# Optimization experiments

Measured on AMD Instinct MI355X. Metric: run time of the kernel, lower is better.

## Reference

```python
import jax, jax.numpy as jnp
import numpy as np

N = 50000
E = 1_000_000
IN_F = 128
NRELA = 128
OUT_F = 128
ALPHA = 0.2  # LeakyReLU negative slope


def setup_inputs() -> dict:
    key = jax.random.key(0)
    k1, k2, k3, k4, k5 = jax.random.split(key, 5)
    inp = {
        "input": jax.random.normal(k1, (N, IN_F), dtype=jnp.float32),
        "edge_embed": jax.random.normal(k2, (E, NRELA), dtype=jnp.float32),
        # xavier_normal-ish scale for the attention params
        "a": jax.random.normal(k3, (OUT_F, 2 * IN_F + NRELA), dtype=jnp.float32) * 0.08,
        "a_2": jax.random.normal(k4, (1, OUT_F), dtype=jnp.float32) * 0.15,
        "edge": jax.random.randint(k5, (2, E), 0, N, dtype=jnp.int64),
    }
    return inp


def reference(input, edge_embed, a, a_2, edge):
    n = input.shape[0]
    src = edge[0]  # aggregation key (row index of sparse tensor)
    dst = edge[1]
    # edge_h: [E, 2*in + nrela]
    edge_h = jnp.concatenate([input[src], input[dst], edge_embed], axis=1)
    # edge_m: [E, out]  (original computes a @ edge_h.T -> [out, E])
    edge_m = edge_h @ a.T
    # powers: [E]
    powers = -jax.nn.leaky_relu(edge_m @ a_2[0], negative_slope=ALPHA)
    edge_e = jnp.exp(powers)  # [E]
    # rowsum over edges sharing the same source node: [N]
    e_rowsum = jax.ops.segment_sum(edge_e, src, num_segments=n)
    e_rowsum = jnp.where(e_rowsum == 0.0, 1e-12, e_rowsum)
    # weighted aggregation: [N, out]
    edge_w = edge_e[:, None] * edge_m
    h_prime = jax.ops.segment_sum(edge_w, src, num_segments=n)
    h_prime = h_prime / e_rowsum[:, None]
    return jax.nn.elu(h_prime)  # concat=True path
```

## Files before the change

### kernel.cpp

```cpp
#include <hip/hip_runtime.h>
#include <math.h>

namespace {

typedef __attribute__((ext_vector_type(8))) short short8;
typedef __attribute__((ext_vector_type(4))) float f32x4;
typedef __attribute__((ext_vector_type(2))) float f2v;

__device__ inline unsigned short f2bf(float x) {
    unsigned u = __float_as_uint(x);
    unsigned r = (u + 0x7FFF + ((u >> 16) & 1)) >> 16;
    return (unsigned short)r;
}

__device__ inline f2v nt2(const f2v* p) { return __builtin_nontemporal_load(p); }
__device__ inline long long ntll(const long long* p) { return __builtin_nontemporal_load(p); }

__device__ inline float wave_sum64(float x) {
    int t;
    t = __builtin_amdgcn_update_dpp(0, __float_as_int(x), 0x111, 0xf, 0xf, true);
    x += __int_as_float(t);
    t = __builtin_amdgcn_update_dpp(0, __float_as_int(x), 0x112, 0xf, 0xf, true);
    x += __int_as_float(t);
    t = __builtin_amdgcn_update_dpp(0, __float_as_int(x), 0x114, 0xf, 0xf, true);
    x += __int_as_float(t);
    t = __builtin_amdgcn_update_dpp(0, __float_as_int(x), 0x118, 0xf, 0xf, true);
    x += __int_as_float(t);
    t = __builtin_amdgcn_update_dpp(0, __float_as_int(x), 0x142, 0xa, 0xf, true);
    x += __int_as_float(t);
    t = __builtin_amdgcn_update_dpp(0, __float_as_int(x), 0x143, 0xc, 0xf, true);
    x += __int_as_float(t);
    return __int_as_float(__builtin_amdgcn_readlane(__float_as_int(x), 63));
}

__global__ void kprep(const int* __restrict__ edge, const float* __restrict__ a,
                      const float* __restrict__ a2, int* __restrict__ flag,
                      unsigned short* __restrict__ Bp12, unsigned short* __restrict__ Bp3,
                      float* __restrict__ w3) {
    int tid = blockIdx.x * blockDim.x + threadIdx.x;
    if (tid < 32768) {
        int j = tid & 7, l = (tid >> 3) & 63, s = (tid >> 9) & 3, f = tid >> 11;
        int col = f * 16 + (l & 15);
        int k = s * 32 + ((l >> 4) << 3) + j;
        float v = (col < 128) ? a[col * 384 + k] : a[(col - 128) * 384 + 128 + k];
        Bp12[tid] = f2bf(v);
    }
    if (tid < 16384) {
        int j = tid & 7, l = (tid >> 3) & 63, s = (tid >> 9) & 3, f = tid >> 11;
        int col = f * 16 + (l & 15);
        int k = s * 32 + ((l >> 4) << 3) + j;
        Bp3[tid] = f2bf(a[col * 384 + 256 + k]);
    }
    if (blockIdx.x == 0 && threadIdx.x < 64) {
        int hw = edge[2 * threadIdx.x + 1];
        unsigned long long b = __ballot(hw == 0);
        if (threadIdx.x == 0) *flag = (b == ~0ull) ? 1 : 0;
    }
    if (blockIdx.x == 1 && threadIdx.x < 128) {
        int k = threadIdx.x;
        float s = 0.f;
        for (int j = 0; j < 128; ++j) s += a2[j] * a[j * 384 + 256 + k];
        w3[k] = s;
    }
}

__global__ __launch_bounds__(256) void kA(const float* __restrict__ input,
                                          const unsigned short* __restrict__ Bp,
                                          const float* __restrict__ a2,
                                          float* __restrict__ U,
                                          unsigned short* __restrict__ Vb,
                                          float* __restrict__ su, float* __restrict__ sv,
                                          const int* __restrict__ edge,
                                          const int* __restrict__ flag,
                                          int* __restrict__ counts,
                                          int n, int E, int nb1) {
    __shared__ char Asb[16384];
    if (blockIdx.x >= nb1) {
        bool is64 = (*flag != 0);
        int half = E >> 1;
        int stride = 1024 * 256;
        for (int i = (blockIdx.x - nb1) * 256 + threadIdx.x; i < half; i += stride) {
            int s0, s1;
            if (is64) { int4 v = ((const int4*)edge)[i]; s0 = v.x; s1 = v.z; }
            else      { int2 v = ((const int2*)edge)[i]; s0 = v.x; s1 = v.y; }
            atomicAdd(&counts[s0], 1);
            atomicAdd(&counts[s1], 1);
        }
        if ((E & 1) && blockIdx.x == nb1 && threadIdx.x == 0) {
            int i = E - 1;
            int s = is64 ? edge[2 * (size_t)i] : edge[i];
            atomicAdd(&counts[s], 1);
        }
        return;
    }
    int tid = threadIdx.x;
    int wid = tid >> 6, lane = tid & 63;
    int rb = blockIdx.x * 64;
    const float4* inp4 = (const float4*)input;
    for (int it = tid; it < 2048; it += 256) {
        int row = it >> 5, c4 = it & 31;
        int gr = rb + row;
        float4 v = make_float4(0.f, 0.f, 0.f, 0.f);
        if (gr < n) v = inp4[(size_t)gr * 32 + c4];
        unsigned long long pk = (unsigned long long)f2bf(v.x) |
                                ((unsigned long long)f2bf(v.y) << 16) |
                                ((unsigned long long)f2bf(v.z) << 32) |
                                ((unsigned long long)f2bf(v.w) << 48);
        int byte = (row * 256 + c4 * 8) ^ ((row & 7) << 4);
        *(unsigned long long*)(Asb + byte) = pk;
    }
    __syncthreads();

    f32x4 acc[16];
    #pragma unroll
    for (int f = 0; f < 16; ++f) acc[f] = (f32x4){0.f, 0.f, 0.f, 0.f};
    const short8* Bf = (const short8*)Bp;
    int arow = (wid << 4) | (lane & 15);
    int abase = arow * 256 + ((lane >> 4) << 4);
    int xorv = (arow & 7) << 4;
    #pragma unroll
    for (int s = 0; s < 4; ++s) {
        short8 af = *(const short8*)(Asb + ((abase + s * 64) ^ xorv));
        #pragma unroll
        for (int f = 0; f < 16; ++f)
            acc[f] = __builtin_amdgcn_mfma_f32_16x16x32_bf16(af, Bf[(f * 4 + s) * 64 + lane],
                                                             acc[f], 0, 0, 0);
    }

    int rloc = (wid << 4) + ((lane >> 4) << 2);
    int cb = lane & 15;
    #pragma unroll
    for (int f = 0; f < 16; ++f) {
        int col = f * 16 + cb;
        #pragma unroll
        for (int reg = 0; reg < 4; ++reg) {
            int r = rb + rloc + reg;
            if (r < n) {
                if (col < 128) U[(size_t)r * 128 + col] = acc[f][reg];
                else           Vb[(size_t)r * 128 + (col - 128)] = f2bf(acc[f][reg]);
            }
        }
    }

    float coef[8];
    #pragma unroll
    for (int f = 0; f < 8; ++f) coef[f] = a2[f * 16 + cb];
    #pragma unroll
    for (int reg = 0; reg < 4; ++reg) {
        float pu = 0.f, pv = 0.f;
        #pragma unroll
        for (int f = 0; f < 8; ++f) {
            pu += acc[f][reg] * coef[f];
            pv += acc[f + 8][reg] * coef[f];
        }
        #pragma unroll
        for (int off = 1; off < 16; off <<= 1) {
            pu += __shfl_xor(pu, off);
            pv += __shfl_xor(pv, off);
        }
        int r = rb + rloc + reg;
        if (cb == 0 && r < n) { su[r] = pu; sv[r] = pv; }
    }
}

__global__ __launch_bounds__(1024) void k3a(int* __restrict__ counts,
                                            int* __restrict__ row_start,
                                            int* __restrict__ partials, int n) {
    __shared__ int wsum[16];
    int tid = threadIdx.x;
    int i = blockIdx.x * 1024 + tid;
    int lane = tid & 63, wv = tid >> 6;
    int v = 0;
    if (i < n) { v = counts[i]; counts[i] = 0; }
    int x = v;
    #pragma unroll
    for (int off = 1; off < 64; off <<= 1) {
        int t = __shfl_up(x, off);
        if (lane >= off) x += t;
    }
    if (lane == 63) wsum[wv] = x;
    __syncthreads();
    if (wv == 0) {
        int ws = (lane < 16) ? wsum[lane] : 0;
        #pragma unroll
        for (int off = 1; off < 16; off <<= 1) {
            int t = __shfl_up(ws, off);
            if (lane >= off) ws += t;
        }
        if (lane < 16) wsum[lane] = ws;
    }
    __syncthreads();
    int woff = (wv > 0) ? wsum[wv - 1] : 0;
    if (i < n) row_start[i] = woff + x - v;
    if (tid == 1023) partials[blockIdx.x] = wsum[15];
}

__global__ void k3b(const int* __restrict__ partials, int* __restrict__ poffs,
                    int* __restrict__ row_start, int nb, int n) {
    int lane = threadIdx.x;
    int carry = 0;
    for (int base = 0; base < nb; base += 64) {
        int v = (base + lane < nb) ? partials[base + lane] : 0;
        int x = v;
        #pragma unroll
        for (int off = 1; off < 64; off <<= 1) {
            int t = __shfl_up(x, off);
            if (lane >= off) x += t;
        }
        if (base + lane < nb) poffs[base + lane] = carry + x - v;
        carry += __shfl(x, 63);
    }
    if (lane == 0) row_start[n] = carry;
}

__global__ void k4_scatter(const int* __restrict__ edge, const int* __restrict__ flag,
                           const int* __restrict__ row_start, const int* __restrict__ poffs,
                           int* __restrict__ counts, long long* __restrict__ epack, int E) {
    bool is64 = (*flag != 0);
    int half = E >> 1;
    int stride = gridDim.x * blockDim.x;
    const int* dbase = edge + (is64 ? 2 * (size_t)E : (size_t)E);
    for (int i = blockIdx.x * blockDim.x + threadIdx.x; i < half; i += stride) {
        int s0, s1, d0, d1;
        if (is64) {
            int4 v = ((const int4*)edge)[i];  s0 = v.x; s1 = v.z;
            int4 w = ((const int4*)dbase)[i]; d0 = w.x; d1 = w.z;
        } else {
            int2 v = ((const int2*)edge)[i];  s0 = v.x; s1 = v.y;
            int2 w = ((const int2*)dbase)[i]; d0 = w.x; d1 = w.y;
        }
        int p0 = row_start[s0] + poffs[s0 >> 10] + atomicAdd(&counts[s0], 1);
        epack[p0] = (long long)(unsigned)(2 * i) | ((long long)(unsigned)d0 << 32);
        int p1 = row_start[s1] + poffs[s1 >> 10] + atomicAdd(&counts[s1], 1);
        epack[p1] = (long long)(unsigned)(2 * i + 1) | ((long long)(unsigned)d1 << 32);
    }
    if ((E & 1) && blockIdx.x == 0 && threadIdx.x == 0) {
        int i = E - 1;
        int s = is64 ? edge[2 * (size_t)i] : edge[i];
        int d = is64 ? dbase[2 * (size_t)i] : dbase[i];
        int pos = row_start[s] + poffs[s >> 10] + atomicAdd(&counts[s], 1);
        epack[pos] = (long long)(unsigned)i | ((long long)(unsigned)d << 32);
    }
}

__global__ __launch_bounds__(256, 3) void k5_agg(const float* __restrict__ edge_embed,
                                                 const unsigned short* __restrict__ Vb,
                                                 const float* __restrict__ su,
                                                 const float* __restrict__ sv,
                                                 const float* __restrict__ w3,
                                                 const int* __restrict__ row_start,
                                                 const int* __restrict__ poffs,
                                                 const long long* __restrict__ epack,
                                                 float* __restrict__ T, float* __restrict__ W,
                                                 float* __restrict__ rowsum, int n) {
    int w = (int)(((size_t)blockIdx.x * blockDim.x + threadIdx.x) >> 6);
    int lane = threadIdx.x & 63;
    if (w >= n) return;
    int start = row_start[w] + poffs[w >> 10];
    int end = (w + 1 < n) ? (row_start[w + 1] + poffs[(w + 1) >> 10]) : row_start[n];
    f2v w3v = ((const f2v*)w3)[lane];
    float su_n = su[w];
    const f2v* EE = (const f2v*)edge_embed;
    const unsigned* VV = (const unsigned*)Vb;
    f2v Tacc = 0.f, Wacc = 0.f;
    float rs = 0.f;
    long long eds[8];
    #pragma unroll
    for (int i = 0; i < 8; ++i)
        eds[i] = (start + i < end) ? ntll(&epack[start + i]) : 0;
    for (int e0 = start; e0 < end; e0 += 8) {
        int nb = end - e0;
        if (nb > 8) nb = 8;
        long long edsn[8];
        #pragma unroll
        for (int i = 0; i < 8; ++i) {
            int idx = e0 + 8 + i;
            edsn[i] = (idx < end) ? ntll(&epack[idx]) : 0;
        }
        f2v emb[8], vv[8];
        float svv[8], part[8];
        #pragma unroll
        for (int i = 0; i < 8; ++i) {
            if (i < nb) {
                int eid = (int)eds[i];
                int dst = (int)(eds[i] >> 32);
                emb[i] = nt2(EE + (size_t)eid * 64 + lane);
                unsigned pv = VV[(size_t)dst * 64 + lane];
                vv[i].x = __uint_as_float(pv << 16);
                vv[i].y = __uint_as_float(pv & 0xffff0000u);
                svv[i] = sv[dst];
            } else {
                emb[i] = 0.f; vv[i] = 0.f; svv[i] = 0.f;
            }
        }
        #pragma unroll
        for (int i = 0; i < 8; ++i)
            part[i] = wave_sum64(emb[i].x * w3v.x + emb[i].y * w3v.y);
        #pragma unroll
        for (int i = 0; i < 8; ++i) {
            if (i < nb) {
                float s = su_n + svv[i] + part[i];
                float lr = (s > 0.f) ? s : 0.2f * s;
                float ee = __expf(-lr);
                rs += ee;
                Tacc += ee * emb[i];
                Wacc += ee * vv[i];
            }
        }
        #pragma unroll
        for (int i = 0; i < 8; ++i) eds[i] = edsn[i];
    }
    ((f2v*)T)[(size_t)w * 64 + lane] = Tacc;
    ((f2v*)W)[(size_t)w * 64 + lane] = Wacc;
    if (lane == 0) rowsum[w] = rs;
}

__global__ __launch_bounds__(256) void k6_mfma(const float* __restrict__ T,
                                               const unsigned short* __restrict__ Bp3,
                                               const float* __restrict__ U,
                                               const float* __restrict__ W,
                                               const float* __restrict__ rowsum,
                                               float* __restrict__ out, int n) {
    __shared__ char Lds[64 * 132 * 4];
    int tid = threadIdx.x;
    int wid = tid >> 6, lane = tid & 63;
    int rb = blockIdx.x * 64;
    const float4* t4 = (const float4*)T;
    for (int it = tid; it < 2048; it += 256) {
        int row = it >> 5, c4 = it & 31;
        int gr = rb + row;
        float4 v = make_float4(0.f, 0.f, 0.f, 0.f);
        if (gr < n) v = t4[(size_t)gr * 32 + c4];
        unsigned long long pk = (unsigned long long)f2bf(v.x) |
                                ((unsigned long long)f2bf(v.y) << 16) |
                                ((unsigned long long)f2bf(v.z) << 32) |
                                ((unsigned long long)f2bf(v.w) << 48);
        int byte = (row * 256 + c4 * 8) ^ ((row & 7) << 4);
        *(unsigned long long*)(Lds + byte) = pk;
    }
    __syncthreads();

    f32x4 acc[8];
    #pragma unroll
    for (int f = 0; f < 8; ++f) acc[f] = (f32x4){0.f, 0.f, 0.f, 0.f};
    const short8* Bf = (const short8*)Bp3;
    int arow = (wid << 4) | (lane & 15);
    int abase = arow * 256 + ((lane >> 4) << 4);
    int xorv = (arow & 7) << 4;
    #pragma unroll
    for (int s = 0; s < 4; ++s) {
        short8 af = *(const short8*)(Lds + ((abase + s * 64) ^ xorv));
        #pragma unroll
        for (int f = 0; f < 8; ++f)
            acc[f] = __builtin_amdgcn_mfma_f32_16x16x32_bf16(af, Bf[(f * 4 + s) * 64 + lane],
                                                             acc[f], 0, 0, 0);
    }
    __syncthreads();

    float* Fs = (float*)Lds;
    int rloc = (wid << 4) + ((lane >> 4) << 2);
    int cb = lane & 15;
    #pragma unroll
    for (int f = 0; f < 8; ++f) {
        #pragma unroll
        for (int reg = 0; reg < 4; ++reg)
            Fs[(rloc + reg) * 132 + f * 16 + cb] = acc[f][reg];
    }
    __syncthreads();

    #pragma unroll
    for (int i = 0; i < 8; ++i) {
        int flat = tid + i * 256;
        int row = flat >> 5, c4 = flat & 31;
        int r = rb + row;
        if (r < n) {
            f32x4 t = *(const f32x4*)&Fs[row * 132 + c4 * 4];
            float rs = rowsum[r];
            f32x4 o;
            if (rs > 0.f) {
                f32x4 u = *(const f32x4*)&U[(size_t)r * 128 + c4 * 4];
                f32x4 w = *(const f32x4*)&W[(size_t)r * 128 + c4 * 4];
                float inv = 1.f / rs;
                float hx = u.x + (t.x + w.x) * inv;
                float hy = u.y + (t.y + w.y) * inv;
                float hz = u.z + (t.z + w.z) * inv;
                float hw = u.w + (t.w + w.w) * inv;
                o.x = (hx > 0.f) ? hx : expm1f(hx);
                o.y = (hy > 0.f) ? hy : expm1f(hy);
                o.z = (hz > 0.f) ? hz : expm1f(hz);
                o.w = (hw > 0.f) ? hw : expm1f(hw);
            } else {
                o = (f32x4){0.f, 0.f, 0.f, 0.f};
            }
            __builtin_nontemporal_store(o, (f32x4*)&out[(size_t)r * 128 + c4 * 4]);
        }
    }
}

}

extern "C" void kernel_launch(void* const* d_in, const int* in_sizes, int n_in,
                              void* d_out, int out_size, void* d_ws, size_t ws_size,
                              hipStream_t stream) {
    const float* input      = (const float*)d_in[0];
    const float* edge_embed = (const float*)d_in[1];
    const float* a          = (const float*)d_in[2];
    const float* a2         = (const float*)d_in[3];
    const int*   edge       = (const int*)d_in[4];
    float* out = (float*)d_out;

    const int n = in_sizes[0] / 128;
    const int E = in_sizes[1] / 128;

    char* p = (char*)d_ws;
    auto carve = [&](size_t bytes) -> char* {
        char* q = p;
        p += (bytes + 255) & ~(size_t)255;
        return q;
    };
    float* U         = (float*)carve((size_t)n * 128 * 4);
    unsigned short* Vb = (unsigned short*)carve((size_t)n * 128 * 2);
    float* T         = (float*)carve((size_t)n * 128 * 4);
    float* W         = (float*)carve((size_t)n * 128 * 4);
    float* su        = (float*)carve((size_t)n * 4);
    float* sv        = (float*)carve((size_t)n * 4);
    float* rowsum    = (float*)carve((size_t)n * 4);
    float* w3        = (float*)carve(128 * 4);
    int*   counts    = (int*)carve((size_t)n * 4);
    int*   row_start = (int*)carve((size_t)(n + 1) * 4);
    long long* epack = (long long*)carve((size_t)E * 8);
    unsigned short* Bp12 = (unsigned short*)carve(32768 * 2);
    unsigned short* Bp3  = (unsigned short*)carve(16384 * 2);
    int*   partials  = (int*)carve(4096 * 4);
    int*   poffs     = (int*)carve(4096 * 4);
    int*   flag      = (int*)carve(4);

    const int NB = (n + 1023) / 1024;
    const int nb1 = (n + 63) / 64;

    hipMemsetAsync(counts, 0, (size_t)n * 4, stream);

    kprep<<<128, 256, 0, stream>>>(edge, a, a2, flag, Bp12, Bp3, w3);
    kA<<<nb1 + 1024, 256, 0, stream>>>(input, Bp12, a2, U, Vb, su, sv,
                                       edge, flag, counts, n, E, nb1);
    k3a<<<NB, 1024, 0, stream>>>(counts, row_start, partials, n);
    k3b<<<1, 64, 0, stream>>>(partials, poffs, row_start, NB, n);
    k4_scatter<<<1024, 256, 0, stream>>>(edge, flag, row_start, poffs, counts, epack, E);
    k5_agg<<<(n + 3) / 4, 256, 0, stream>>>(edge_embed, Vb, su, sv, w3,
                                            row_start, poffs, epack, T, W, rowsum, n);
    k6_mfma<<<(n + 63) / 64, 256, 0, stream>>>(T, Bp3, U, W, rowsum, out, n);
}
```

Baseline: 373.4 us.

## Store only edge ids in CSR; gather dst from edge array with deeper prefetch

The scatter kernel now writes a 4-byte edge id per CSR slot instead of a packed 8-byte (id,dst) pair. It also stops reading the dst half of the edge array and uses nontemporal stores. The aggregation kernel then looks up dst through an extra dependent gather into the original edge array. To hide that added indirection it prefetches ids two batches ahead and dst one batch ahead. This trades scatter write and read bandwidth for random gathers in the aggregation loop and more registers.

```diff
diff --git a/kernel.cpp b/kernel.cpp
--- a/kernel.cpp
+++ b/kernel.cpp
@@ -14,7 +14,7 @@
 }
 
 __device__ inline f2v nt2(const f2v* p) { return __builtin_nontemporal_load(p); }
-__device__ inline long long ntll(const long long* p) { return __builtin_nontemporal_load(p); }
+__device__ inline int ntl(const int* p) { return __builtin_nontemporal_load(p); }
 
 __device__ inline float wave_sum64(float x) {
     int t;
@@ -215,31 +215,24 @@
 
 __global__ void k4_scatter(const int* __restrict__ edge, const int* __restrict__ flag,
                            const int* __restrict__ row_start, const int* __restrict__ poffs,
-                           int* __restrict__ counts, long long* __restrict__ epack, int E) {
+                           int* __restrict__ counts, int* __restrict__ eidx, int E) {
     bool is64 = (*flag != 0);
     int half = E >> 1;
     int stride = gridDim.x * blockDim.x;
-    const int* dbase = edge + (is64 ? 2 * (size_t)E : (size_t)E);
     for (int i = blockIdx.x * blockDim.x + threadIdx.x; i < half; i += stride) {
-        int s0, s1, d0, d1;
-        if (is64) {
-            int4 v = ((const int4*)edge)[i];  s0 = v.x; s1 = v.z;
-            int4 w = ((const int4*)dbase)[i]; d0 = w.x; d1 = w.z;
-        } else {
-            int2 v = ((const int2*)edge)[i];  s0 = v.x; s1 = v.y;
-            int2 w = ((const int2*)dbase)[i]; d0 = w.x; d1 = w.y;
-        }
+        int s0, s1;
+        if (is64) { int4 v = ((const int4*)edge)[i]; s0 = v.x; s1 = v.z; }
+        else      { int2 v = ((const int2*)edge)[i]; s0 = v.x; s1 = v.y; }
         int p0 = row_start[s0] + poffs[s0 >> 10] + atomicAdd(&counts[s0], 1);
-        epack[p0] = (long long)(unsigned)(2 * i) | ((long long)(unsigned)d0 << 32);
+        __builtin_nontemporal_store(2 * i, &eidx[p0]);
         int p1 = row_start[s1] + poffs[s1 >> 10] + atomicAdd(&counts[s1], 1);
-        epack[p1] = (long long)(unsigned)(2 * i + 1) | ((long long)(unsigned)d1 << 32);
+        __builtin_nontemporal_store(2 * i + 1, &eidx[p1]);
     }
     if ((E & 1) && blockIdx.x == 0 && threadIdx.x == 0) {
         int i = E - 1;
         int s = is64 ? edge[2 * (size_t)i] : edge[i];
-        int d = is64 ? dbase[2 * (size_t)i] : dbase[i];
         int pos = row_start[s] + poffs[s >> 10] + atomicAdd(&counts[s], 1);
-        epack[pos] = (long long)(unsigned)i | ((long long)(unsigned)d << 32);
+        __builtin_nontemporal_store(i, &eidx[pos]);
     }
 }
 
@@ -250,9 +243,11 @@
                                                  const float* __restrict__ w3,
                                                  const int* __restrict__ row_start,
                                                  const int* __restrict__ poffs,
-                                                 const long long* __restrict__ epack,
+                                                 const int* __restrict__ eidx,
+                                                 const int* __restrict__ edge,
+                                                 const int* __restrict__ flag,
                                                  float* __restrict__ T, float* __restrict__ W,
-                                                 float* __restrict__ rowsum, int n) {
+                                                 float* __restrict__ rowsum, int n, int E) {
     int w = (int)(((size_t)blockIdx.x * blockDim.x + threadIdx.x) >> 6);
     int lane = threadIdx.x & 63;
     if (w >= n) return;
@@ -262,33 +257,42 @@
     float su_n = su[w];
     const f2v* EE = (const f2v*)edge_embed;
     const unsigned* VV = (const unsigned*)Vb;
+    bool is64 = (*flag != 0);
+    const int* dstb = edge + (is64 ? 2 * (size_t)E : (size_t)E);
+    int dsh = is64 ? 1 : 0;
     f2v Tacc = 0.f, Wacc = 0.f;
     float rs = 0.f;
-    long long eds[8];
+    int e0v[8], e1v[8], d0v[8];
+    #pragma unroll
+    for (int i = 0; i < 8; ++i) {
+        e0v[i] = (start + i < end) ? ntl(&eidx[start + i]) : 0;
+        e1v[i] = (start + 8 + i < end) ? ntl(&eidx[start + 8 + i]) : 0;
+    }
     #pragma unroll
     for (int i = 0; i < 8; ++i)
-        eds[i] = (start + i < end) ? ntll(&epack[start + i]) : 0;
-    for (int e0 = start; e0 < end; e0 += 8) {
-        int nb = end - e0;
+        d0v[i] = dstb[(size_t)((unsigned)e0v[i]) << dsh];
+    for (int b0 = start; b0 < end; b0 += 8) {
+        int nb = end - b0;
         if (nb > 8) nb = 8;
-        long long edsn[8];
+        int e2v[8], d1v[8];
         #pragma unroll
         for (int i = 0; i < 8; ++i) {
-            int idx = e0 + 8 + i;
-            edsn[i] = (idx < end) ? ntll(&epack[idx]) : 0;
-        }
+            int idx = b0 + 16 + i;
+            e2v[i] = (idx < end) ? ntl(&eidx[idx]) : 0;
+        }
+        #pragma unroll
+        for (int i = 0; i < 8; ++i)
+            d1v[i] = dstb[(size_t)((unsigned)e1v[i]) << dsh];
         f2v emb[8], vv[8];
         float svv[8], part[8];
         #pragma unroll
         for (int i = 0; i < 8; ++i) {
             if (i < nb) {
-                int eid = (int)eds[i];
-                int dst = (int)(eds[i] >> 32);
-                emb[i] = nt2(EE + (size_t)eid * 64 + lane);
-                unsigned pv = VV[(size_t)dst * 64 + lane];
+                emb[i] = nt2(EE + (size_t)((unsigned)e0v[i]) * 64 + lane);
+                unsigned pv = VV[(size_t)((unsigned)d0v[i]) * 64 + lane];
                 vv[i].x = __uint_as_float(pv << 16);
                 vv[i].y = __uint_as_float(pv & 0xffff0000u);
-                svv[i] = sv[dst];
+                svv[i] = sv[d0v[i]];
             } else {
                 emb[i] = 0.f; vv[i] = 0.f; svv[i] = 0.f;
             }
@@ -308,7 +312,7 @@
             }
         }
         #pragma unroll
-        for (int i = 0; i < 8; ++i) eds[i] = edsn[i];
+        for (int i = 0; i < 8; ++i) { e0v[i] = e1v[i]; e1v[i] = e2v[i]; d0v[i] = d1v[i]; }
     }
     ((f2v*)T)[(size_t)w * 64 + lane] = Tacc;
     ((f2v*)W)[(size_t)w * 64 + lane] = Wacc;
@@ -428,7 +432,7 @@
     float* w3        = (float*)carve(128 * 4);
     int*   counts    = (int*)carve((size_t)n * 4);
     int*   row_start = (int*)carve((size_t)(n + 1) * 4);
-    long long* epack = (long long*)carve((size_t)E * 8);
+    int*   eidx      = (int*)carve((size_t)E * 4);
     unsigned short* Bp12 = (unsigned short*)carve(32768 * 2);
     unsigned short* Bp3  = (unsigned short*)carve(16384 * 2);
     int*   partials  = (int*)carve(4096 * 4);
@@ -445,8 +449,9 @@
                                        edge, flag, counts, n, E, nb1);
     k3a<<<NB, 1024, 0, stream>>>(counts, row_start, partials, n);
     k3b<<<1, 64, 0, stream>>>(partials, poffs, row_start, NB, n);
-    k4_scatter<<<1024, 256, 0, stream>>>(edge, flag, row_start, poffs, counts, epack, E);
+    k4_scatter<<<1024, 256, 0, stream>>>(edge, flag, row_start, poffs, counts, eidx, E);
     k5_agg<<<(n + 3) / 4, 256, 0, stream>>>(edge_embed, Vb, su, sv, w3,
-                                            row_start, poffs, epack, T, W, rowsum, n);
+                                            row_start, poffs, eidx, edge, flag,
+                                            T, W, rowsum, n, E);
     k6_mfma<<<(n + 63) / 64, 256, 0, stream>>>(T, Bp3, U, W, rowsum, out, n);
 }
```

Result: slower. 425.5 us (+14.0%).

## Process 8 edges per wave concurrently with 16-lane groups in aggregation

Applied to the files above, without the earlier changes.

The aggregation kernel now splits each wave into four 16-lane groups. Each group handles a different edge, so eight edges are covered per iteration in two slots, and each lane loads 32-byte vectors of the edge embedding and the bf16 V row. The per-edge dot product is reduced with a 16-lane DPP row reduction instead of a full 64-lane reduction plus readlane. Partial accumulators are combined across groups with shuffles at the end. This cuts reduction overhead and issues wider loads, but it drops the software prefetch of edge indices and the occupancy hint.

```diff
diff --git a/kernel.cpp b/kernel.cpp
--- a/kernel.cpp
+++ b/kernel.cpp
@@ -5,6 +5,7 @@
 
 typedef __attribute__((ext_vector_type(8))) short short8;
 typedef __attribute__((ext_vector_type(4))) float f32x4;
+typedef __attribute__((ext_vector_type(4))) unsigned u32x4;
 typedef __attribute__((ext_vector_type(2))) float f2v;
 
 __device__ inline unsigned short f2bf(float x) {
@@ -13,24 +14,21 @@
     return (unsigned short)r;
 }
 
-__device__ inline f2v nt2(const f2v* p) { return __builtin_nontemporal_load(p); }
-__device__ inline long long ntll(const long long* p) { return __builtin_nontemporal_load(p); }
-
-__device__ inline float wave_sum64(float x) {
+__device__ inline f32x4 nt4(const f32x4* p) { return __builtin_nontemporal_load(p); }
+__device__ inline float bfl(unsigned u) { return __uint_as_float(u << 16); }
+__device__ inline float bfh(unsigned u) { return __uint_as_float(u & 0xffff0000u); }
+
+__device__ inline float row_allsum16(float x) {
     int t;
-    t = __builtin_amdgcn_update_dpp(0, __float_as_int(x), 0x111, 0xf, 0xf, true);
+    t = __builtin_amdgcn_update_dpp(0, __float_as_int(x), 0x128, 0xf, 0xf, true);
     x += __int_as_float(t);
-    t = __builtin_amdgcn_update_dpp(0, __float_as_int(x), 0x112, 0xf, 0xf, true);
+    t = __builtin_amdgcn_update_dpp(0, __float_as_int(x), 0x124, 0xf, 0xf, true);
     x += __int_as_float(t);
-    t = __builtin_amdgcn_update_dpp(0, __float_as_int(x), 0x114, 0xf, 0xf, true);
+    t = __builtin_amdgcn_update_dpp(0, __float_as_int(x), 0x122, 0xf, 0xf, true);
     x += __int_as_float(t);
-    t = __builtin_amdgcn_update_dpp(0, __float_as_int(x), 0x118, 0xf, 0xf, true);
+    t = __builtin_amdgcn_update_dpp(0, __float_as_int(x), 0x121, 0xf, 0xf, true);
     x += __int_as_float(t);
-    t = __builtin_amdgcn_update_dpp(0, __float_as_int(x), 0x142, 0xa, 0xf, true);
-    x += __int_as_float(t);
-    t = __builtin_amdgcn_update_dpp(0, __float_as_int(x), 0x143, 0xc, 0xf, true);
-    x += __int_as_float(t);
-    return __int_as_float(__builtin_amdgcn_readlane(__float_as_int(x), 63));
+    return x;
 }
 
 __global__ void kprep(const int* __restrict__ edge, const float* __restrict__ a,
@@ -243,75 +241,78 @@
     }
 }
 
-__global__ __launch_bounds__(256, 3) void k5_agg(const float* __restrict__ edge_embed,
-                                                 const unsigned short* __restrict__ Vb,
-                                                 const float* __restrict__ su,
-                                                 const float* __restrict__ sv,
-                                                 const float* __restrict__ w3,
-                                                 const int* __restrict__ row_start,
-                                                 const int* __restrict__ poffs,
-                                                 const long long* __restrict__ epack,
-                                                 float* __restrict__ T, float* __restrict__ W,
-                                                 float* __restrict__ rowsum, int n) {
+__global__ __launch_bounds__(256) void k5_agg(const float* __restrict__ edge_embed,
+                                              const unsigned short* __restrict__ Vb,
+                                              const float* __restrict__ su,
+                                              const float* __restrict__ sv,
+                                              const float* __restrict__ w3,
+                                              const int* __restrict__ row_start,
+                                              const int* __restrict__ poffs,
+                                              const long long* __restrict__ epack,
+                                              float* __restrict__ T, float* __restrict__ W,
+                                              float* __restrict__ rowsum, int n) {
     int w = (int)(((size_t)blockIdx.x * blockDim.x + threadIdx.x) >> 6);
     int lane = threadIdx.x & 63;
     if (w >= n) return;
+    int g = lane >> 4, j = lane & 15;
     int start = row_start[w] + poffs[w >> 10];
     int end = (w + 1 < n) ? (row_start[w + 1] + poffs[(w + 1) >> 10]) : row_start[n];
-    f2v w3v = ((const f2v*)w3)[lane];
+    const f32x4* EE4 = (const f32x4*)edge_embed;
+    f32x4 w3a = ((const f32x4*)w3)[j * 2];
+    f32x4 w3b = ((const f32x4*)w3)[j * 2 + 1];
     float su_n = su[w];
-    const f2v* EE = (const f2v*)edge_embed;
-    const unsigned* VV = (const unsigned*)Vb;
-    f2v Tacc = 0.f, Wacc = 0.f;
+    f32x4 Ta = 0.f, Tb = 0.f, Wa = 0.f, Wb = 0.f;
     float rs = 0.f;
-    long long eds[8];
-    #pragma unroll
-    for (int i = 0; i < 8; ++i)
-        eds[i] = (start + i < end) ? ntll(&epack[start + i]) : 0;
     for (int e0 = start; e0 < end; e0 += 8) {
-        int nb = end - e0;
-        if (nb > 8) nb = 8;
-        long long edsn[8];
-        #pragma unroll
-        for (int i = 0; i < 8; ++i) {
-            int idx = e0 + 8 + i;
-            edsn[i] = (idx < end) ? ntll(&epack[idx]) : 0;
-        }
-        f2v emb[8], vv[8];
-        float svv[8], part[8];
-        #pragma unroll
-        for (int i = 0; i < 8; ++i) {
-            if (i < nb) {
-                int eid = (int)eds[i];
-                int dst = (int)(eds[i] >> 32);
-                emb[i] = nt2(EE + (size_t)eid * 64 + lane);
-                unsigned pv = VV[(size_t)dst * 64 + lane];
-                vv[i].x = __uint_as_float(pv << 16);
-                vv[i].y = __uint_as_float(pv & 0xffff0000u);
-                svv[i] = sv[dst];
-            } else {
-                emb[i] = 0.f; vv[i] = 0.f; svv[i] = 0.f;
-            }
-        }
-        #pragma unroll
-        for (int i = 0; i < 8; ++i)
-            part[i] = wave_sum64(emb[i].x * w3v.x + emb[i].y * w3v.y);
-        #pragma unroll
-        for (int i = 0; i < 8; ++i) {
-            if (i < nb) {
-                float s = su_n + svv[i] + part[i];
-                float lr = (s > 0.f) ? s : 0.2f * s;
-                float ee = __expf(-lr);
-                rs += ee;
-                Tacc += ee * emb[i];
-                Wacc += ee * vv[i];
-            }
-        }
-        #pragma unroll
-        for (int i = 0; i < 8; ++i) eds[i] = edsn[i];
-    }
-    ((f2v*)T)[(size_t)w * 64 + lane] = Tacc;
-    ((f2v*)W)[(size_t)w * 64 + lane] = Wacc;
+        int ia = e0 + g, ib = e0 + 4 + g;
+        bool va = ia < end, vb = ib < end;
+        long long eda = va ? epack[ia] : 0;
+        long long edb = vb ? epack[ib] : 0;
+        int eida = (int)eda, dsta = (int)(eda >> 32);
+        int eidb = (int)edb, dstb = (int)(edb >> 32);
+        f32x4 ea0 = nt4(EE4 + (size_t)eida * 32 + j * 2);
+        f32x4 ea1 = nt4(EE4 + (size_t)eida * 32 + j * 2 + 1);
+        f32x4 eb0 = nt4(EE4 + (size_t)eidb * 32 + j * 2);
+        f32x4 eb1 = nt4(EE4 + (size_t)eidb * 32 + j * 2 + 1);
+        u32x4 vua = *(const u32x4*)(Vb + (size_t)dsta * 128 + j * 8);
+        u32x4 vub = *(const u32x4*)(Vb + (size_t)dstb * 128 + j * 8);
+        float sva = sv[dsta], svb = sv[dstb];
+        float pa = ea0.x * w3a.x + ea0.y * w3a.y + ea0.z * w3a.z + ea0.w * w3a.w +
+                   ea1.x * w3b.x + ea1.y * w3b.y + ea1.z * w3b.z + ea1.w * w3b.w;
+        float pb = eb0.x * w3a.x + eb0.y * w3a.y + eb0.z * w3a.z + eb0.w * w3a.w +
+                   eb1.x * w3b.x + eb1.y * w3b.y + eb1.z * w3b.z + eb1.w * w3b.w;
+        pa = row_allsum16(pa);
+        pb = row_allsum16(pb);
+        float sa = su_n + sva + pa;
+        float sb = su_n + svb + pb;
+        float la = (sa > 0.f) ? sa : 0.2f * sa;
+        float lb = (sb > 0.f) ? sb : 0.2f * sb;
+        float eea = va ? __expf(-la) : 0.f;
+        float eeb = vb ? __expf(-lb) : 0.f;
+        rs += eea + eeb;
+        Ta += eea * ea0; Tb += eea * ea1;
+        Ta += eeb * eb0; Tb += eeb * eb1;
+        f32x4 vfa0 = {bfl(vua.x), bfh(vua.x), bfl(vua.y), bfh(vua.y)};
+        f32x4 vfa1 = {bfl(vua.z), bfh(vua.z), bfl(vua.w), bfh(vua.w)};
+        f32x4 vfb0 = {bfl(vub.x), bfh(vub.x), bfl(vub.y), bfh(vub.y)};
+        f32x4 vfb1 = {bfl(vub.z), bfh(vub.z), bfl(vub.w), bfh(vub.w)};
+        Wa += eea * vfa0; Wb += eea * vfa1;
+        Wa += eeb * vfb0; Wb += eeb * vfb1;
+    }
+    #pragma unroll
+    for (int k = 0; k < 4; ++k) {
+        Ta[k] += __shfl_xor(Ta[k], 16); Ta[k] += __shfl_xor(Ta[k], 32);
+        Tb[k] += __shfl_xor(Tb[k], 16); Tb[k] += __shfl_xor(Tb[k], 32);
+        Wa[k] += __shfl_xor(Wa[k], 16); Wa[k] += __shfl_xor(Wa[k], 32);
+        Wb[k] += __shfl_xor(Wb[k], 16); Wb[k] += __shfl_xor(Wb[k], 32);
+    }
+    rs += __shfl_xor(rs, 16); rs += __shfl_xor(rs, 32);
+    if (g == 0) {
+        ((f32x4*)T)[(size_t)w * 32 + j * 2] = Ta;
+        ((f32x4*)T)[(size_t)w * 32 + j * 2 + 1] = Tb;
+        ((f32x4*)W)[(size_t)w * 32 + j * 2] = Wa;
+        ((f32x4*)W)[(size_t)w * 32 + j * 2 + 1] = Wb;
+    }
     if (lane == 0) rowsum[w] = rs;
 }
 
```

Measured after the change: 311.1 us (median of 2 runs). -16.7%, faster.
